# Optimization experiments

Measured on AMD Instinct MI355X. Metric: run time of the kernel, lower is better.

Reference implementation:

```python
import jax, jax.numpy as jnp
import numpy as np

EMB = 1024
HEAD = 128

def setup_inputs() -> dict:
    key = jax.random.key(0)
    kx, kk, kq, kv = jax.random.split(key, 4)
    s = 1.0 / np.sqrt(EMB)
    return {
        "x": jax.random.normal(kx, (8, 2048, EMB), dtype=jnp.float32),
        "Wk": jax.random.normal(kk, (EMB, HEAD), dtype=jnp.float32) * s,
        "Wq": jax.random.normal(kq, (EMB, HEAD), dtype=jnp.float32) * s,
        "Wv": jax.random.normal(kv, (EMB, HEAD), dtype=jnp.float32) * s,
    }

def reference(x, Wk, Wq, Wv):
    # x: [B,T,E]; projections (no bias)
    k = jnp.einsum('bte,eh->bth', x, Wk)
    q = jnp.einsum('bte,eh->bth', x, Wq)
    v = jnp.einsum('bte,eh->bth', x, Wv)
    # scores: [B,T,T], NOTE: no 1/sqrt(d) scaling in original module
    qk = jnp.einsum('bih,bjh->bij', q, k)
    T = x.shape[1]
    causal = jnp.tril(jnp.ones((T, T), dtype=bool))  # True = keep
    qk = jnp.where(causal, qk, -jnp.inf)
    # NOTE: softmax over axis -2 (query axis), as in original
    attn = jax.nn.softmax(qk, axis=-2)
    return jnp.einsum('bij,bjh->bih', attn, v)
```

## Files before the change

kernel.cpp:

```cpp
#include <hip/hip_runtime.h>

typedef unsigned short u16;
typedef unsigned int u32;
typedef _Float16 f16;
typedef __attribute__((ext_vector_type(8))) _Float16 f16x8;
typedef __attribute__((ext_vector_type(4))) float f32x4;

constexpr int SEQ = 2048;
constexpr int EMBD = 1024;
constexpr int HD = 128;
constexpr int NB = 8;
constexpr int NSL = 8;

__device__ inline u16 f2h(float f) {
  f16 h = (f16)f;
  return __builtin_bit_cast(u16, h);
}
__device__ inline u32 pack2(float a, float b) {
  return (u32)f2h(a) | ((u32)f2h(b) << 16);
}

__device__ inline f32x4 mfma16(f16x8 a, f16x8 b, f32x4 c) {
  return __builtin_amdgcn_mfma_f32_16x16x32_f16(a, b, c, 0, 0, 0);
}

template<int R, int C>
__device__ inline void stage_tile(u16* lds, const u16* __restrict__ g, int ldg) {
  constexpr int CH = (R * C) / (8 * 256);
  int t = threadIdx.x;
#pragma unroll
  for (int ch = 0; ch < CH; ++ch) {
    int lin = ch * 256 + t;
    int row = lin / (C / 8);
    int cc = lin % (C / 8);
    int byte = row * (C * 2) + cc * 16;
    byte ^= (row & 7) << 4;
    *reinterpret_cast<uint4*>(reinterpret_cast<char*>(lds) + byte) =
        *reinterpret_cast<const uint4*>(g + (size_t)row * ldg + cc * 8);
  }
}

template<int R, int C>
__device__ inline void stage_tile_f32(u16* lds, const float* __restrict__ g, int ldg) {
  constexpr int CH = (R * C) / (8 * 256);
  int t = threadIdx.x;
#pragma unroll
  for (int ch = 0; ch < CH; ++ch) {
    int lin = ch * 256 + t;
    int row = lin / (C / 8);
    int cc = lin % (C / 8);
    const float* p = g + (size_t)row * ldg + cc * 8;
    float4 a = *reinterpret_cast<const float4*>(p);
    float4 b = *reinterpret_cast<const float4*>(p + 4);
    uint4 o;
    o.x = pack2(a.x, a.y);
    o.y = pack2(a.z, a.w);
    o.z = pack2(b.x, b.y);
    o.w = pack2(b.z, b.w);
    int byte = row * (C * 2) + cc * 16;
    byte ^= (row & 7) << 4;
    *reinterpret_cast<uint4*>(reinterpret_cast<char*>(lds) + byte) = o;
  }
}

template<int RB>
__device__ inline f16x8 frag_ld(const u16* lds, int row, int elem) {
  int byte = row * RB + elem * 2;
  byte ^= (row & 7) << 4;
  return *reinterpret_cast<const f16x8*>(reinterpret_cast<const char*>(lds) + byte);
}

__global__ __launch_bounds__(256) void k_cvt_w(const float* __restrict__ Wq,
                                               const float* __restrict__ Wk,
                                               const float* __restrict__ Wv,
                                               u16* __restrict__ Wt) {
  int t = blockIdx.x * 256 + threadIdx.x;
  int e0 = (t & 255) * 4;
  int h = (t >> 8) & 127;
  int w = t >> 15;
  const float* W = (w == 0) ? Wq : (w == 1) ? Wk : Wv;
  ushort4 o;
  o.x = f2h(W[(size_t)(e0 + 0) * HD + h]);
  o.y = f2h(W[(size_t)(e0 + 1) * HD + h]);
  o.z = f2h(W[(size_t)(e0 + 2) * HD + h]);
  o.w = f2h(W[(size_t)(e0 + 3) * HD + h]);
  *reinterpret_cast<ushort4*>(Wt + ((size_t)w * HD + h) * EMBD + e0) = o;
}

__global__ __launch_bounds__(256, 2) void k_proj(const float* __restrict__ x,
                                                 const u16* __restrict__ Wt,
                                                 u16* __restrict__ Qb,
                                                 u16* __restrict__ Kb,
                                                 u16* __restrict__ Vtb) {
  __shared__ __align__(16) u16 As[32 * 64];
  __shared__ __align__(16) u16 Bs[3][128 * 64];
  const int mt = blockIdx.x;
  const int lane = threadIdx.x & 63, wave = threadIdx.x >> 6;
  const int rh = wave & 1, fq = wave >> 1;
  f32x4 zero = {0.f, 0.f, 0.f, 0.f};
  f32x4 acc[3][4];
#pragma unroll
  for (int w = 0; w < 3; w++)
#pragma unroll
    for (int f = 0; f < 4; f++) acc[w][f] = zero;

  for (int k0 = 0; k0 < EMBD; k0 += 64) {
    __syncthreads();
    stage_tile_f32<32, 64>(As, x + (size_t)mt * 32 * EMBD + k0, EMBD);
    stage_tile<128, 64>(Bs[0], Wt + 0 * HD * EMBD + k0, EMBD);
    stage_tile<128, 64>(Bs[1], Wt + 1 * (size_t)HD * EMBD + k0, EMBD);
    stage_tile<128, 64>(Bs[2], Wt + 2 * (size_t)HD * EMBD + k0, EMBD);
    __syncthreads();
#pragma unroll
    for (int kk = 0; kk < 2; kk++) {
      f16x8 af = frag_ld<128>(As, rh * 16 + (lane & 15), kk * 32 + (lane >> 4) * 8);
#pragma unroll
      for (int w = 0; w < 3; w++)
#pragma unroll
        for (int f = 0; f < 4; f++) {
          f16x8 bw = frag_ld<128>(Bs[w], (fq * 4 + f) * 16 + (lane & 15),
                                  kk * 32 + (lane >> 4) * 8);
          acc[w][f] = mfma16(af, bw, acc[w][f]);
        }
    }
  }
#pragma unroll
  for (int w = 0; w < 2; w++) {
    u16* P = w ? Kb : Qb;
#pragma unroll
    for (int f = 0; f < 4; f++)
#pragma unroll
      for (int r = 0; r < 4; r++) {
        int i = mt * 32 + rh * 16 + (lane >> 4) * 4 + r;
        int h = (fq * 4 + f) * 16 + (lane & 15);
        P[(size_t)i * HD + h] = f2h(acc[w][f][r]);
      }
  }
  {
    int bb = (mt * 32) >> 11;
    int t0 = (mt * 32) & 2047;
#pragma unroll
    for (int f = 0; f < 4; f++) {
      int h = (fq * 4 + f) * 16 + (lane & 15);
      int t = t0 + rh * 16 + (lane >> 4) * 4;
      ushort4 o;
      o.x = f2h(acc[2][f][0]);
      o.y = f2h(acc[2][f][1]);
      o.z = f2h(acc[2][f][2]);
      o.w = f2h(acc[2][f][3]);
      *reinterpret_cast<ushort4*>(Vtb + ((size_t)bb * HD + h) * SEQ + t) = o;
    }
  }
}

__device__ inline void merge_ml(float& m, float& l, float m2, float l2) {
  float mn = fmaxf(m, m2);
  float a = (m > -1e37f) ? l * __expf(m - mn) : 0.f;
  float b = (m2 > -1e37f) ? l2 * __expf(m2 - mn) : 0.f;
  m = mn;
  l = a + b;
}

__global__ __launch_bounds__(256, 2) void k_statsA(const u16* __restrict__ Qb,
                                                   const u16* __restrict__ Kb,
                                                   float* __restrict__ mpart,
                                                   float* __restrict__ lpart) {
  __shared__ __align__(16) u16 Tile[128 * 128];
  const int id = blockIdx.y * 64 + blockIdx.x;
  const int bb = id & 7;
  const int z = (id >> 3) & 7, sl = id >> 6;
  const int lane = threadIdx.x & 63, wave = threadIdx.x >> 6, wj = wave * 32;
  f32x4 zero = {0.f, 0.f, 0.f, 0.f};

  for (int ph = 0; ph < 2; ph++) {
    const int jt = ph ? (15 - z) : z;
    __syncthreads();
    stage_tile<128, 128>(Tile, Kb + ((size_t)bb * SEQ + jt * 128) * HD, HD);
    __syncthreads();
    f16x8 af[2][4];
#pragma unroll
    for (int fj = 0; fj < 2; fj++)
#pragma unroll
      for (int kk = 0; kk < 4; kk++)
        af[fj][kk] = frag_ld<256>(Tile, wj + fj * 16 + (lane & 15), kk * 32 + (lane >> 4) * 8);
    float m[2][4], l[2][4];
#pragma unroll
    for (int a = 0; a < 2; a++)
#pragma unroll
      for (int r = 0; r < 4; r++) {
        m[a][r] = -INFINITY;
        l[a][r] = 0.f;
      }
    int it0 = jt + ((sl - jt) & 7);
    for (int it = it0; it < 16; it += 8) {
      __syncthreads();
      stage_tile<128, 128>(Tile, Qb + ((size_t)bb * SEQ + it * 128) * HD, HD);
      __syncthreads();
      f32x4 acc[2][8];
#pragma unroll
      for (int a = 0; a < 2; a++)
#pragma unroll
        for (int b = 0; b < 8; b++) acc[a][b] = zero;
#pragma unroll
      for (int kk = 0; kk < 4; kk++)
#pragma unroll
        for (int fi = 0; fi < 8; fi++) {
          f16x8 bq = frag_ld<256>(Tile, fi * 16 + (lane & 15), kk * 32 + (lane >> 4) * 8);
          acc[0][fi] = mfma16(af[0][kk], bq, acc[0][fi]);
          acc[1][fi] = mfma16(af[1][kk], bq, acc[1][fi]);
        }
#pragma unroll
      for (int fj = 0; fj < 2; fj++)
#pragma unroll
        for (int r = 0; r < 4; r++) {
          int jg = jt * 128 + wj + fj * 16 + (lane >> 4) * 4 + r;
          float v[8];
          float vmax = -INFINITY;
#pragma unroll
          for (int fi = 0; fi < 8; fi++) {
            int ig = it * 128 + fi * 16 + (lane & 15);
            v[fi] = (ig >= jg) ? acc[fj][fi][r] : -INFINITY;
            vmax = fmaxf(vmax, v[fi]);
          }
          if (vmax > -1e37f) {
            float mn = fmaxf(m[fj][r], vmax);
            float sc = (m[fj][r] > -1e37f) ? __expf(m[fj][r] - mn) : 0.f;
            float ss = 0.f;
#pragma unroll
            for (int fi = 0; fi < 8; fi++)
              ss += (v[fi] > -1e37f) ? __expf(v[fi] - mn) : 0.f;
            l[fj][r] = l[fj][r] * sc + ss;
            m[fj][r] = mn;
          }
        }
    }
#pragma unroll
    for (int fj = 0; fj < 2; fj++)
#pragma unroll
      for (int r = 0; r < 4; r++)
        for (int msk = 1; msk <= 8; msk <<= 1) {
          float m2 = __shfl_xor(m[fj][r], msk);
          float l2 = __shfl_xor(l[fj][r], msk);
          merge_ml(m[fj][r], l[fj][r], m2, l2);
        }
    if ((lane & 15) == 0) {
#pragma unroll
      for (int fj = 0; fj < 2; fj++)
#pragma unroll
        for (int r = 0; r < 4; r++) {
          int j = jt * 128 + wj + fj * 16 + (lane >> 4) * 4 + r;
          size_t idx = (size_t)sl * (NB * SEQ) + (size_t)bb * SEQ + j;
          mpart[idx] = m[fj][r];
          lpart[idx] = l[fj][r];
        }
    }
  }
}

__global__ __launch_bounds__(256) void k_stats_reduce(const float* __restrict__ mpart,
                                                      const float* __restrict__ lpart,
                                                      float* __restrict__ Mg,
                                                      float* __restrict__ RLg) {
  int idx = blockIdx.x * 256 + threadIdx.x;
  float m = -INFINITY;
#pragma unroll
  for (int sl = 0; sl < NSL; sl++) m = fmaxf(m, mpart[sl * (NB * SEQ) + idx]);
  float l = 0.f;
#pragma unroll
  for (int sl = 0; sl < NSL; sl++) {
    float ms = mpart[sl * (NB * SEQ) + idx];
    if (ms > -1e37f) l += lpart[sl * (NB * SEQ) + idx] * __expf(ms - m);
  }
  Mg[idx] = m;
  RLg[idx] = 1.0f / l;
}

__global__ __launch_bounds__(256, 2) void k_passB(const u16* __restrict__ Qb,
                                                  const u16* __restrict__ Kb,
                                                  const u16* __restrict__ Vtb,
                                                  const float* __restrict__ Mg,
                                                  const float* __restrict__ RLg,
                                                  u16* __restrict__ opart) {
  __shared__ __align__(16) u16 Ks[64 * 128];
  __shared__ __align__(16) u16 Vs[128 * 64];
  __shared__ __align__(16) u16 Ps[128 * 64];
  __shared__ float sm[64];
  __shared__ float srl[64];
  const int id = blockIdx.y * 64 + blockIdx.x;
  const int bb = id & 7;
  const int z = (id >> 3) & 7, sl = id >> 6;
  const int lane = threadIdx.x & 63, wave = threadIdx.x >> 6, wi = wave * 32;
  f32x4 zero = {0.f, 0.f, 0.f, 0.f};

  for (int ph = 0; ph < 2; ph++) {
    const int it = ph ? (15 - z) : z;
    f16x8 qf[2][4];
#pragma unroll
    for (int fi = 0; fi < 2; fi++)
#pragma unroll
      for (int kk = 0; kk < 4; kk++) {
        size_t row = (size_t)bb * SEQ + it * 128 + wi + fi * 16 + (lane & 15);
        qf[fi][kk] = *reinterpret_cast<const f16x8*>(Qb + row * HD + kk * 32 + (lane >> 4) * 8);
      }
    f32x4 accO[2][8];
#pragma unroll
    for (int a = 0; a < 2; a++)
#pragma unroll
      for (int b = 0; b < 8; b++) accO[a][b] = zero;

    for (int jt = sl; jt <= 2 * it + 1; jt += 8) {
      __syncthreads();
      stage_tile<64, 128>(Ks, Kb + ((size_t)bb * SEQ + jt * 64) * HD, HD);
      stage_tile<128, 64>(Vs, Vtb + (size_t)bb * HD * SEQ + jt * 64, SEQ);
      if (threadIdx.x < 64)
        sm[threadIdx.x] = Mg[bb * SEQ + jt * 64 + threadIdx.x];
      else if (threadIdx.x < 128)
        srl[threadIdx.x - 64] = RLg[bb * SEQ + jt * 64 + threadIdx.x - 64];
      __syncthreads();
      f32x4 accS[2][4];
#pragma unroll
      for (int a = 0; a < 2; a++)
#pragma unroll
        for (int b = 0; b < 4; b++) accS[a][b] = zero;
#pragma unroll
      for (int kk = 0; kk < 4; kk++)
#pragma unroll
        for (int fj = 0; fj < 4; fj++) {
          f16x8 bk = frag_ld<256>(Ks, fj * 16 + (lane & 15), kk * 32 + (lane >> 4) * 8);
          accS[0][fj] = mfma16(qf[0][kk], bk, accS[0][fj]);
          accS[1][fj] = mfma16(qf[1][kk], bk, accS[1][fj]);
        }
#pragma unroll
      for (int fi = 0; fi < 2; fi++)
#pragma unroll
        for (int fj = 0; fj < 4; fj++) {
          int jloc = fj * 16 + (lane & 15);
          float mj = sm[jloc], rlj = srl[jloc];
          int jg = jt * 64 + jloc;
#pragma unroll
          for (int r = 0; r < 4; r++) {
            int iloc = wi + fi * 16 + (lane >> 4) * 4 + r;
            int ig = it * 128 + iloc;
            float p = __expf(accS[fi][fj][r] - mj) * rlj;
            if (ig < jg) p = 0.f;
            int byte = iloc * 128 + jloc * 2;
            byte ^= (iloc & 7) << 4;
            *reinterpret_cast<u16*>(reinterpret_cast<char*>(Ps) + byte) = f2h(p);
          }
        }
      __syncthreads();
#pragma unroll
      for (int kk = 0; kk < 2; kk++) {
        f16x8 pa0 = frag_ld<128>(Ps, wi + (lane & 15), kk * 32 + (lane >> 4) * 8);
        f16x8 pa1 = frag_ld<128>(Ps, wi + 16 + (lane & 15), kk * 32 + (lane >> 4) * 8);
#pragma unroll
        for (int fh = 0; fh < 8; fh++) {
          f16x8 bv = frag_ld<128>(Vs, fh * 16 + (lane & 15), kk * 32 + (lane >> 4) * 8);
          accO[0][fh] = mfma16(pa0, bv, accO[0][fh]);
          accO[1][fh] = mfma16(pa1, bv, accO[1][fh]);
        }
      }
    }
#pragma unroll
    for (int fi = 0; fi < 2; fi++)
#pragma unroll
      for (int fh = 0; fh < 8; fh++)
#pragma unroll
        for (int r = 0; r < 4; r++) {
          int ig = it * 128 + wi + fi * 16 + (lane >> 4) * 4 + r;
          int h = fh * 16 + (lane & 15);
          opart[(((size_t)sl * NB + bb) * SEQ + ig) * HD + h] = f2h(accO[fi][fh][r]);
        }
  }
}

__global__ __launch_bounds__(256) void k_reduceB(const u16* __restrict__ opart,
                                                 float* __restrict__ out) {
  size_t base = ((size_t)blockIdx.x * 256 + threadIdx.x) * 8;
  const size_t S = (size_t)NB * SEQ * HD;
  float s[8];
#pragma unroll
  for (int j = 0; j < 8; j++) s[j] = 0.f;
#pragma unroll
  for (int sl = 0; sl < NSL; sl++) {
    f16x8 v = *reinterpret_cast<const f16x8*>(opart + sl * S + base);
#pragma unroll
    for (int j = 0; j < 8; j++) s[j] += (float)v[j];
  }
  float4 o0 = {s[0], s[1], s[2], s[3]};
  float4 o1 = {s[4], s[5], s[6], s[7]};
  *reinterpret_cast<float4*>(out + base) = o0;
  *reinterpret_cast<float4*>(out + base + 4) = o1;
}

extern "C" void kernel_launch(void* const* d_in, const int* in_sizes, int n_in,
                              void* d_out, int out_size, void* d_ws, size_t ws_size,
                              hipStream_t stream) {
  (void)in_sizes; (void)n_in; (void)out_size; (void)ws_size;
  const float* x = (const float*)d_in[0];
  const float* Wk = (const float*)d_in[1];
  const float* Wq = (const float*)d_in[2];
  const float* Wv = (const float*)d_in[3];
  float* out = (float*)d_out;
  char* ws = (char*)d_ws;

  u16* Wt = (u16*)(ws + 0);
  u16* Qb = (u16*)(ws + 786432);
  u16* Kb = (u16*)(ws + 4980736);
  u16* Vtb = (u16*)(ws + 9175040);
  float* mpart = (float*)(ws + 13369344);
  float* lpart = (float*)(ws + 13893632);
  float* Mg = (float*)(ws + 14417920);
  float* RLg = (float*)(ws + 14483456);
  u16* opart = (u16*)(ws + 14548992);

  k_cvt_w<<<384, 256, 0, stream>>>(Wq, Wk, Wv, Wt);
  k_proj<<<512, 256, 0, stream>>>(x, Wt, Qb, Kb, Vtb);
  k_statsA<<<dim3(64, 8), 256, 0, stream>>>(Qb, Kb, mpart, lpart);
  k_stats_reduce<<<64, 256, 0, stream>>>(mpart, lpart, Mg, RLg);
  k_passB<<<dim3(64, 8), 256, 0, stream>>>(Qb, Kb, Vtb, Mg, RLg, opart);
  k_reduceB<<<1024, 256, 0, stream>>>(opart, out);
}
```

Measured before the change: 95.25 us.

## Pre-swizzle Q/K/V/W layouts and double-buffer tiles with direct global-to-LDS loads

The projection weights, Q, K and the transposed V are now written to global memory already in the XOR-swizzled tile layout. This lets the projection, stats and output-pass kernels copy tiles into LDS with global_load_lds instead of going through registers. Each of those three kernels now double-buffers its tiles, so the next tile is prefetched while MFMAs run on the current one. The projection kernel gets a new 512-thread, 2D-grid tiling, and passB reuses the K buffer as the P scratch and reads the row stats straight from global. The risks are higher LDS use per block, lower occupancy, and a layout contract that every kernel must read consistently.

```diff
diff --git a/kernel.cpp b/kernel.cpp
--- a/kernel.cpp
+++ b/kernel.cpp
@@ -12,61 +12,22 @@
 constexpr int NB = 8;
 constexpr int NSL = 8;
 
-__device__ inline u16 f2h(float f) {
-  f16 h = (f16)f;
-  return __builtin_bit_cast(u16, h);
-}
-__device__ inline u32 pack2(float a, float b) {
-  return (u32)f2h(a) | ((u32)f2h(b) << 16);
-}
+__device__ inline u16 f2h(float f) { return __builtin_bit_cast(u16, (f16)f); }
+__device__ inline u32 pack2(float a, float b) { return (u32)f2h(a) | ((u32)f2h(b) << 16); }
 
 __device__ inline f32x4 mfma16(f16x8 a, f16x8 b, f32x4 c) {
   return __builtin_amdgcn_mfma_f32_16x16x32_f16(a, b, c, 0, 0, 0);
 }
 
-template<int R, int C>
-__device__ inline void stage_tile(u16* lds, const u16* __restrict__ g, int ldg) {
-  constexpr int CH = (R * C) / (8 * 256);
-  int t = threadIdx.x;
-#pragma unroll
-  for (int ch = 0; ch < CH; ++ch) {
-    int lin = ch * 256 + t;
-    int row = lin / (C / 8);
-    int cc = lin % (C / 8);
-    int byte = row * (C * 2) + cc * 16;
-    byte ^= (row & 7) << 4;
-    *reinterpret_cast<uint4*>(reinterpret_cast<char*>(lds) + byte) =
-        *reinterpret_cast<const uint4*>(g + (size_t)row * ldg + cc * 8);
-  }
-}
-
-template<int R, int C>
-__device__ inline void stage_tile_f32(u16* lds, const float* __restrict__ g, int ldg) {
-  constexpr int CH = (R * C) / (8 * 256);
-  int t = threadIdx.x;
-#pragma unroll
-  for (int ch = 0; ch < CH; ++ch) {
-    int lin = ch * 256 + t;
-    int row = lin / (C / 8);
-    int cc = lin % (C / 8);
-    const float* p = g + (size_t)row * ldg + cc * 8;
-    float4 a = *reinterpret_cast<const float4*>(p);
-    float4 b = *reinterpret_cast<const float4*>(p + 4);
-    uint4 o;
-    o.x = pack2(a.x, a.y);
-    o.y = pack2(a.z, a.w);
-    o.z = pack2(b.x, b.y);
-    o.w = pack2(b.z, b.w);
-    int byte = row * (C * 2) + cc * 16;
-    byte ^= (row & 7) << 4;
-    *reinterpret_cast<uint4*>(reinterpret_cast<char*>(lds) + byte) = o;
-  }
+__device__ __forceinline__ void gload16(const u16* g, u16* l) {
+  __builtin_amdgcn_global_load_lds(
+      (const __attribute__((address_space(1))) u32*)g,
+      (__attribute__((address_space(3))) u32*)l, 16, 0, 0);
 }
 
 template<int RB>
-__device__ inline f16x8 frag_ld(const u16* lds, int row, int elem) {
-  int byte = row * RB + elem * 2;
-  byte ^= (row & 7) << 4;
+__device__ inline f16x8 frag_ld(const u16* lds, int row, int e) {
+  int byte = row * RB + ((e * 2) ^ ((row & 7) << 4));
   return *reinterpret_cast<const f16x8*>(reinterpret_cast<const char*>(lds) + byte);
 }
 
@@ -76,81 +37,104 @@
                                                u16* __restrict__ Wt) {
   int t = blockIdx.x * 256 + threadIdx.x;
   int e0 = (t & 255) * 4;
-  int h = (t >> 8) & 127;
-  int w = t >> 15;
+  int H = t >> 8;
+  int w = H >> 7, h = H & 127;
   const float* W = (w == 0) ? Wq : (w == 1) ? Wk : Wv;
   ushort4 o;
   o.x = f2h(W[(size_t)(e0 + 0) * HD + h]);
   o.y = f2h(W[(size_t)(e0 + 1) * HD + h]);
   o.z = f2h(W[(size_t)(e0 + 2) * HD + h]);
   o.w = f2h(W[(size_t)(e0 + 3) * HD + h]);
-  *reinterpret_cast<ushort4*>(Wt + ((size_t)w * HD + h) * EMBD + e0) = o;
-}
-
-__global__ __launch_bounds__(256, 2) void k_proj(const float* __restrict__ x,
+  int k0t = e0 >> 6, ec = e0 & 63;
+  size_t el = (size_t)(k0t * 384 + H) * 64 + (ec ^ ((H & 7) << 3));
+  *reinterpret_cast<ushort4*>(Wt + el) = o;
+}
+
+__global__ __launch_bounds__(512, 4) void k_proj(const float* __restrict__ x,
                                                  const u16* __restrict__ Wt,
                                                  u16* __restrict__ Qb,
                                                  u16* __restrict__ Kb,
                                                  u16* __restrict__ Vtb) {
-  __shared__ __align__(16) u16 As[32 * 64];
-  __shared__ __align__(16) u16 Bs[3][128 * 64];
-  const int mt = blockIdx.x;
-  const int lane = threadIdx.x & 63, wave = threadIdx.x >> 6;
-  const int rh = wave & 1, fq = wave >> 1;
+  __shared__ __align__(16) u16 As[2][64 * 64];
+  __shared__ __align__(16) u16 Bs[2][192 * 64];
+  const int mt = blockIdx.x, ny = blockIdx.y;
+  const int t = threadIdx.x, lane = t & 63, wave = t >> 6;
+  const int rh = (wave & 1) * 32, cq = (wave >> 1) * 48;
+  const int ar = t >> 3, ac = t & 7;
+  const float* asrc = x + (size_t)(mt * 64 + ar) * EMBD + ac * 8;
+  const int adst = ar * 64 + ((ac * 8) ^ ((ar & 7) << 3));
   f32x4 zero = {0.f, 0.f, 0.f, 0.f};
-  f32x4 acc[3][4];
-#pragma unroll
-  for (int w = 0; w < 3; w++)
-#pragma unroll
-    for (int f = 0; f < 4; f++) acc[w][f] = zero;
-
-  for (int k0 = 0; k0 < EMBD; k0 += 64) {
+  f32x4 acc[2][3];
+#pragma unroll
+  for (int a = 0; a < 2; ++a)
+#pragma unroll
+    for (int b = 0; b < 3; ++b) acc[a][b] = zero;
+
+  {
+#pragma unroll
+    for (int q = 0; q < 3; ++q) {
+      int lin = q * 512 + t;
+      gload16(Wt + ny * 12288 + lin * 8, &Bs[0][lin * 8]);
+    }
+    float4 a0 = *reinterpret_cast<const float4*>(asrc);
+    float4 a1 = *reinterpret_cast<const float4*>(asrc + 4);
+    uint4 o = {pack2(a0.x, a0.y), pack2(a0.z, a0.w), pack2(a1.x, a1.y), pack2(a1.z, a1.w)};
+    *reinterpret_cast<uint4*>(&As[0][adst]) = o;
+  }
+  __syncthreads();
+  int cur = 0;
+  for (int s = 0; s < 16; ++s) {
+    float4 a0, a1;
+    const bool pf = (s < 15);
+    if (pf) {
+#pragma unroll
+      for (int q = 0; q < 3; ++q) {
+        int lin = q * 512 + t;
+        gload16(Wt + (s + 1) * 24576 + ny * 12288 + lin * 8, &Bs[cur ^ 1][lin * 8]);
+      }
+      a0 = *reinterpret_cast<const float4*>(asrc + (s + 1) * 64);
+      a1 = *reinterpret_cast<const float4*>(asrc + (s + 1) * 64 + 4);
+    }
+#pragma unroll
+    for (int kk = 0; kk < 2; ++kk) {
+      f16x8 af0 = frag_ld<128>(As[cur], rh + (lane & 15), kk * 32 + (lane >> 4) * 8);
+      f16x8 af1 = frag_ld<128>(As[cur], rh + 16 + (lane & 15), kk * 32 + (lane >> 4) * 8);
+#pragma unroll
+      for (int fc = 0; fc < 3; ++fc) {
+        f16x8 bw = frag_ld<128>(Bs[cur], cq + fc * 16 + (lane & 15), kk * 32 + (lane >> 4) * 8);
+        acc[0][fc] = mfma16(af0, bw, acc[0][fc]);
+        acc[1][fc] = mfma16(af1, bw, acc[1][fc]);
+      }
+    }
+    if (pf) {
+      uint4 o = {pack2(a0.x, a0.y), pack2(a0.z, a0.w), pack2(a1.x, a1.y), pack2(a1.z, a1.w)};
+      *reinterpret_cast<uint4*>(&As[cur ^ 1][adst]) = o;
+    }
     __syncthreads();
-    stage_tile_f32<32, 64>(As, x + (size_t)mt * 32 * EMBD + k0, EMBD);
-    stage_tile<128, 64>(Bs[0], Wt + 0 * HD * EMBD + k0, EMBD);
-    stage_tile<128, 64>(Bs[1], Wt + 1 * (size_t)HD * EMBD + k0, EMBD);
-    stage_tile<128, 64>(Bs[2], Wt + 2 * (size_t)HD * EMBD + k0, EMBD);
-    __syncthreads();
-#pragma unroll
-    for (int kk = 0; kk < 2; kk++) {
-      f16x8 af = frag_ld<128>(As, rh * 16 + (lane & 15), kk * 32 + (lane >> 4) * 8);
-#pragma unroll
-      for (int w = 0; w < 3; w++)
-#pragma unroll
-        for (int f = 0; f < 4; f++) {
-          f16x8 bw = frag_ld<128>(Bs[w], (fq * 4 + f) * 16 + (lane & 15),
-                                  kk * 32 + (lane >> 4) * 8);
-          acc[w][f] = mfma16(af, bw, acc[w][f]);
-        }
-    }
-  }
-#pragma unroll
-  for (int w = 0; w < 2; w++) {
-    u16* P = w ? Kb : Qb;
-#pragma unroll
-    for (int f = 0; f < 4; f++)
-#pragma unroll
-      for (int r = 0; r < 4; r++) {
-        int i = mt * 32 + rh * 16 + (lane >> 4) * 4 + r;
-        int h = (fq * 4 + f) * 16 + (lane & 15);
-        P[(size_t)i * HD + h] = f2h(acc[w][f][r]);
-      }
-  }
-  {
-    int bb = (mt * 32) >> 11;
-    int t0 = (mt * 32) & 2047;
-#pragma unroll
-    for (int f = 0; f < 4; f++) {
-      int h = (fq * 4 + f) * 16 + (lane & 15);
-      int t = t0 + rh * 16 + (lane >> 4) * 4;
-      ushort4 o;
-      o.x = f2h(acc[2][f][0]);
-      o.y = f2h(acc[2][f][1]);
-      o.z = f2h(acc[2][f][2]);
-      o.w = f2h(acc[2][f][3]);
-      *reinterpret_cast<ushort4*>(Vtb + ((size_t)bb * HD + h) * SEQ + t) = o;
-    }
-  }
+    cur ^= 1;
+  }
+#pragma unroll
+  for (int fi = 0; fi < 2; ++fi)
+#pragma unroll
+    for (int fc = 0; fc < 3; ++fc) {
+      int gcol = ny * 192 + cq + fc * 16 + (lane & 15);
+      int w = gcol >> 7, h = gcol & 127;
+      int i0 = mt * 64 + rh + fi * 16 + (lane >> 4) * 4;
+      if (w < 2) {
+        u16* P = w ? Kb : Qb;
+#pragma unroll
+        for (int r = 0; r < 4; ++r) {
+          int i = i0 + r;
+          P[(size_t)i * 128 + (h ^ ((i & 7) << 3))] = f2h(acc[fi][fc][r]);
+        }
+      } else {
+        int bb = i0 >> 11, jt = (i0 >> 6) & 31, tl = i0 & 63;
+        ushort4 o = {f2h(acc[fi][fc][0]), f2h(acc[fi][fc][1]),
+                     f2h(acc[fi][fc][2]), f2h(acc[fi][fc][3])};
+        size_t el = ((size_t)(bb * 32 + jt) * 128 + h) * 64 + (tl ^ ((h & 7) << 3));
+        *reinterpret_cast<ushort4*>(Vtb + el) = o;
+      }
+    }
 }
 
 __device__ inline void merge_ml(float& m, float& l, float m2, float l2) {
@@ -165,79 +149,97 @@
                                                    const u16* __restrict__ Kb,
                                                    float* __restrict__ mpart,
                                                    float* __restrict__ lpart) {
-  __shared__ __align__(16) u16 Tile[128 * 128];
+  __shared__ __align__(16) u16 Qs[2][128 * 128];
   const int id = blockIdx.y * 64 + blockIdx.x;
-  const int bb = id & 7;
-  const int z = (id >> 3) & 7, sl = id >> 6;
-  const int lane = threadIdx.x & 63, wave = threadIdx.x >> 6, wj = wave * 32;
+  const int bb = id & 7, z = (id >> 3) & 7, sl = id >> 6;
+  const int t = threadIdx.x, lane = t & 63, wj = (t >> 6) * 32;
   f32x4 zero = {0.f, 0.f, 0.f, 0.f};
 
-  for (int ph = 0; ph < 2; ph++) {
-    const int jt = ph ? (15 - z) : z;
+  for (int ph = 0; ph < 2; ++ph) {
+    const int jt = ph ? 15 - z : z;
     __syncthreads();
-    stage_tile<128, 128>(Tile, Kb + ((size_t)bb * SEQ + jt * 128) * HD, HD);
+#pragma unroll
+    for (int q = 0; q < 8; ++q) {
+      int lin = q * 256 + t;
+      gload16(Kb + ((size_t)bb * SEQ + jt * 128) * 128 + lin * 8, &Qs[0][lin * 8]);
+    }
     __syncthreads();
     f16x8 af[2][4];
 #pragma unroll
-    for (int fj = 0; fj < 2; fj++)
-#pragma unroll
-      for (int kk = 0; kk < 4; kk++)
-        af[fj][kk] = frag_ld<256>(Tile, wj + fj * 16 + (lane & 15), kk * 32 + (lane >> 4) * 8);
+    for (int fj = 0; fj < 2; ++fj)
+#pragma unroll
+      for (int kk = 0; kk < 4; ++kk)
+        af[fj][kk] = frag_ld<256>(Qs[0], wj + fj * 16 + (lane & 15), kk * 32 + (lane >> 4) * 8);
     float m[2][4], l[2][4];
 #pragma unroll
-    for (int a = 0; a < 2; a++)
-#pragma unroll
-      for (int r = 0; r < 4; r++) {
+    for (int a = 0; a < 2; ++a)
+#pragma unroll
+      for (int r = 0; r < 4; ++r) {
         m[a][r] = -INFINITY;
         l[a][r] = 0.f;
       }
-    int it0 = jt + ((sl - jt) & 7);
-    for (int it = it0; it < 16; it += 8) {
-      __syncthreads();
-      stage_tile<128, 128>(Tile, Qb + ((size_t)bb * SEQ + it * 128) * HD, HD);
-      __syncthreads();
-      f32x4 acc[2][8];
-#pragma unroll
-      for (int a = 0; a < 2; a++)
-#pragma unroll
-        for (int b = 0; b < 8; b++) acc[a][b] = zero;
-#pragma unroll
-      for (int kk = 0; kk < 4; kk++)
-#pragma unroll
-        for (int fi = 0; fi < 8; fi++) {
-          f16x8 bq = frag_ld<256>(Tile, fi * 16 + (lane & 15), kk * 32 + (lane >> 4) * 8);
-          acc[0][fi] = mfma16(af[0][kk], bq, acc[0][fi]);
-          acc[1][fi] = mfma16(af[1][kk], bq, acc[1][fi]);
-        }
-#pragma unroll
-      for (int fj = 0; fj < 2; fj++)
-#pragma unroll
-        for (int r = 0; r < 4; r++) {
-          int jg = jt * 128 + wj + fj * 16 + (lane >> 4) * 4 + r;
-          float v[8];
-          float vmax = -INFINITY;
-#pragma unroll
-          for (int fi = 0; fi < 8; fi++) {
-            int ig = it * 128 + fi * 16 + (lane & 15);
-            v[fi] = (ig >= jg) ? acc[fj][fi][r] : -INFINITY;
-            vmax = fmaxf(vmax, v[fi]);
+    const int it0 = jt + ((sl - jt) & 7);
+    int cur = 1;
+    if (it0 < 16) {
+#pragma unroll
+      for (int q = 0; q < 8; ++q) {
+        int lin = q * 256 + t;
+        gload16(Qb + ((size_t)bb * SEQ + it0 * 128) * 128 + lin * 8, &Qs[1][lin * 8]);
+      }
+      for (int it = it0; it < 16; it += 8) {
+        __syncthreads();
+        if (it + 8 < 16) {
+#pragma unroll
+          for (int q = 0; q < 8; ++q) {
+            int lin = q * 256 + t;
+            gload16(Qb + ((size_t)bb * SEQ + (it + 8) * 128) * 128 + lin * 8,
+                    &Qs[cur ^ 1][lin * 8]);
           }
-          if (vmax > -1e37f) {
-            float mn = fmaxf(m[fj][r], vmax);
-            float sc = (m[fj][r] > -1e37f) ? __expf(m[fj][r] - mn) : 0.f;
-            float ss = 0.f;
-#pragma unroll
-            for (int fi = 0; fi < 8; fi++)
-              ss += (v[fi] > -1e37f) ? __expf(v[fi] - mn) : 0.f;
-            l[fj][r] = l[fj][r] * sc + ss;
-            m[fj][r] = mn;
+        }
+        f32x4 acc[2][8];
+#pragma unroll
+        for (int a = 0; a < 2; ++a)
+#pragma unroll
+          for (int b = 0; b < 8; ++b) acc[a][b] = zero;
+#pragma unroll
+        for (int kk = 0; kk < 4; ++kk)
+#pragma unroll
+          for (int fi = 0; fi < 8; ++fi) {
+            f16x8 bq = frag_ld<256>(Qs[cur], fi * 16 + (lane & 15), kk * 32 + (lane >> 4) * 8);
+            acc[0][fi] = mfma16(af[0][kk], bq, acc[0][fi]);
+            acc[1][fi] = mfma16(af[1][kk], bq, acc[1][fi]);
           }
-        }
-    }
-#pragma unroll
-    for (int fj = 0; fj < 2; fj++)
-#pragma unroll
-      for (int r = 0; r < 4; r++)
+#pragma unroll
+        for (int fj = 0; fj < 2; ++fj)
+#pragma unroll
+          for (int r = 0; r < 4; ++r) {
+            int jg = jt * 128 + wj + fj * 16 + (lane >> 4) * 4 + r;
+            float v[8];
+            float vmax = -INFINITY;
+#pragma unroll
+            for (int fi = 0; fi < 8; ++fi) {
+              int ig = it * 128 + fi * 16 + (lane & 15);
+              v[fi] = (ig >= jg) ? acc[fj][fi][r] : -INFINITY;
+              vmax = fmaxf(vmax, v[fi]);
+            }
+            if (vmax > -1e37f) {
+              float mn = fmaxf(m[fj][r], vmax);
+              float sc = (m[fj][r] > -1e37f) ? __expf(m[fj][r] - mn) : 0.f;
+              float ss = 0.f;
+#pragma unroll
+              for (int fi = 0; fi < 8; ++fi)
+                ss += (v[fi] > -1e37f) ? __expf(v[fi] - mn) : 0.f;
+              l[fj][r] = l[fj][r] * sc + ss;
+              m[fj][r] = mn;
+            }
+          }
+        cur ^= 1;
+      }
+    }
+#pragma unroll
+    for (int fj = 0; fj < 2; ++fj)
+#pragma unroll
+      for (int r = 0; r < 4; ++r)
         for (int msk = 1; msk <= 8; msk <<= 1) {
           float m2 = __shfl_xor(m[fj][r], msk);
           float l2 = __shfl_xor(l[fj][r], msk);
@@ -245,9 +247,9 @@
         }
     if ((lane & 15) == 0) {
 #pragma unroll
-      for (int fj = 0; fj < 2; fj++)
-#pragma unroll
-        for (int r = 0; r < 4; r++) {
+      for (int fj = 0; fj < 2; ++fj)
+#pragma unroll
+        for (int r = 0; r < 4; ++r) {
           int j = jt * 128 + wj + fj * 16 + (lane >> 4) * 4 + r;
           size_t idx = (size_t)sl * (NB * SEQ) + (size_t)bb * SEQ + j;
           mpart[idx] = m[fj][r];
@@ -281,92 +283,106 @@
                                                   const float* __restrict__ Mg,
                                                   const float* __restrict__ RLg,
                                                   u16* __restrict__ opart) {
-  __shared__ __align__(16) u16 Ks[64 * 128];
-  __shared__ __align__(16) u16 Vs[128 * 64];
-  __shared__ __align__(16) u16 Ps[128 * 64];
-  __shared__ float sm[64];
-  __shared__ float srl[64];
+  __shared__ __align__(16) u16 Ks2[2][64 * 128];
+  __shared__ __align__(16) u16 Vs2[2][128 * 64];
   const int id = blockIdx.y * 64 + blockIdx.x;
-  const int bb = id & 7;
-  const int z = (id >> 3) & 7, sl = id >> 6;
-  const int lane = threadIdx.x & 63, wave = threadIdx.x >> 6, wi = wave * 32;
+  const int bb = id & 7, z = (id >> 3) & 7, sl = id >> 6;
+  const int t = threadIdx.x, lane = t & 63, wi = (t >> 6) * 32;
   f32x4 zero = {0.f, 0.f, 0.f, 0.f};
 
-  for (int ph = 0; ph < 2; ph++) {
-    const int it = ph ? (15 - z) : z;
+  auto stageKV = [&](int jt, int b) {
+#pragma unroll
+    for (int q = 0; q < 4; ++q) {
+      int lin = q * 256 + t;
+      gload16(Kb + ((size_t)bb * SEQ + jt * 64) * 128 + lin * 8, &Ks2[b][lin * 8]);
+    }
+#pragma unroll
+    for (int q = 0; q < 4; ++q) {
+      int lin = q * 256 + t;
+      gload16(Vtb + ((size_t)bb * 32 + jt) * 8192 + lin * 8, &Vs2[b][lin * 8]);
+    }
+  };
+
+  for (int ph = 0; ph < 2; ++ph) {
+    const int it = ph ? 15 - z : z;
     f16x8 qf[2][4];
 #pragma unroll
-    for (int fi = 0; fi < 2; fi++)
-#pragma unroll
-      for (int kk = 0; kk < 4; kk++) {
-        size_t row = (size_t)bb * SEQ + it * 128 + wi + fi * 16 + (lane & 15);
-        qf[fi][kk] = *reinterpret_cast<const f16x8*>(Qb + row * HD + kk * 32 + (lane >> 4) * 8);
+    for (int fi = 0; fi < 2; ++fi)
+#pragma unroll
+      for (int kk = 0; kk < 4; ++kk) {
+        size_t gi = (size_t)bb * SEQ + it * 128 + wi + fi * 16 + (lane & 15);
+        int e0 = kk * 32 + (lane >> 4) * 8;
+        qf[fi][kk] = *reinterpret_cast<const f16x8*>(Qb + gi * 128 + (e0 ^ (((int)gi & 7) << 3)));
       }
     f32x4 accO[2][8];
 #pragma unroll
-    for (int a = 0; a < 2; a++)
-#pragma unroll
-      for (int b = 0; b < 8; b++) accO[a][b] = zero;
-
-    for (int jt = sl; jt <= 2 * it + 1; jt += 8) {
+    for (int a = 0; a < 2; ++a)
+#pragma unroll
+      for (int b = 0; b < 8; ++b) accO[a][b] = zero;
+    const int jtmax = 2 * it + 1;
+    int cur = 0;
+    __syncthreads();
+    if (sl <= jtmax) stageKV(sl, 0);
+    for (int jt = sl; jt <= jtmax; jt += 8) {
       __syncthreads();
-      stage_tile<64, 128>(Ks, Kb + ((size_t)bb * SEQ + jt * 64) * HD, HD);
-      stage_tile<128, 64>(Vs, Vtb + (size_t)bb * HD * SEQ + jt * 64, SEQ);
-      if (threadIdx.x < 64)
-        sm[threadIdx.x] = Mg[bb * SEQ + jt * 64 + threadIdx.x];
-      else if (threadIdx.x < 128)
-        srl[threadIdx.x - 64] = RLg[bb * SEQ + jt * 64 + threadIdx.x - 64];
-      __syncthreads();
+      float mjv[4], rlv[4];
+#pragma unroll
+      for (int fj = 0; fj < 4; ++fj) {
+        int jg = jt * 64 + fj * 16 + (lane & 15);
+        mjv[fj] = Mg[bb * SEQ + jg];
+        rlv[fj] = RLg[bb * SEQ + jg];
+      }
       f32x4 accS[2][4];
 #pragma unroll
-      for (int a = 0; a < 2; a++)
-#pragma unroll
-        for (int b = 0; b < 4; b++) accS[a][b] = zero;
-#pragma unroll
-      for (int kk = 0; kk < 4; kk++)
-#pragma unroll
-        for (int fj = 0; fj < 4; fj++) {
-          f16x8 bk = frag_ld<256>(Ks, fj * 16 + (lane & 15), kk * 32 + (lane >> 4) * 8);
+      for (int a = 0; a < 2; ++a)
+#pragma unroll
+        for (int b = 0; b < 4; ++b) accS[a][b] = zero;
+#pragma unroll
+      for (int kk = 0; kk < 4; ++kk)
+#pragma unroll
+        for (int fj = 0; fj < 4; ++fj) {
+          f16x8 bk = frag_ld<256>(Ks2[cur], fj * 16 + (lane & 15), kk * 32 + (lane >> 4) * 8);
           accS[0][fj] = mfma16(qf[0][kk], bk, accS[0][fj]);
           accS[1][fj] = mfma16(qf[1][kk], bk, accS[1][fj]);
         }
-#pragma unroll
-      for (int fi = 0; fi < 2; fi++)
-#pragma unroll
-        for (int fj = 0; fj < 4; fj++) {
-          int jloc = fj * 16 + (lane & 15);
-          float mj = sm[jloc], rlj = srl[jloc];
-          int jg = jt * 64 + jloc;
-#pragma unroll
-          for (int r = 0; r < 4; r++) {
+      __syncthreads();
+      if (jt + 8 <= jtmax) stageKV(jt + 8, cur ^ 1);
+      u16* Ps = Ks2[cur];
+#pragma unroll
+      for (int fj = 0; fj < 4; ++fj) {
+        int jloc = fj * 16 + (lane & 15);
+        int jg = jt * 64 + jloc;
+        float mj = mjv[fj], rlj = rlv[fj];
+#pragma unroll
+        for (int fi = 0; fi < 2; ++fi)
+#pragma unroll
+          for (int r = 0; r < 4; ++r) {
             int iloc = wi + fi * 16 + (lane >> 4) * 4 + r;
             int ig = it * 128 + iloc;
             float p = __expf(accS[fi][fj][r] - mj) * rlj;
             if (ig < jg) p = 0.f;
-            int byte = iloc * 128 + jloc * 2;
-            byte ^= (iloc & 7) << 4;
-            *reinterpret_cast<u16*>(reinterpret_cast<char*>(Ps) + byte) = f2h(p);
+            Ps[iloc * 64 + (jloc ^ ((iloc & 7) << 3))] = f2h(p);
           }
-        }
-      __syncthreads();
-#pragma unroll
-      for (int kk = 0; kk < 2; kk++) {
-        f16x8 pa0 = frag_ld<128>(Ps, wi + (lane & 15), kk * 32 + (lane >> 4) * 8);
-        f16x8 pa1 = frag_ld<128>(Ps, wi + 16 + (lane & 15), kk * 32 + (lane >> 4) * 8);
-#pragma unroll
-        for (int fh = 0; fh < 8; fh++) {
-          f16x8 bv = frag_ld<128>(Vs, fh * 16 + (lane & 15), kk * 32 + (lane >> 4) * 8);
+      }
+#pragma unroll
+      for (int ks = 0; ks < 2; ++ks) {
+        f16x8 pa0 = frag_ld<128>(Ps, wi + (lane & 15), ks * 32 + (lane >> 4) * 8);
+        f16x8 pa1 = frag_ld<128>(Ps, wi + 16 + (lane & 15), ks * 32 + (lane >> 4) * 8);
+#pragma unroll
+        for (int fh = 0; fh < 8; ++fh) {
+          f16x8 bv = frag_ld<128>(Vs2[cur], fh * 16 + (lane & 15), ks * 32 + (lane >> 4) * 8);
           accO[0][fh] = mfma16(pa0, bv, accO[0][fh]);
           accO[1][fh] = mfma16(pa1, bv, accO[1][fh]);
         }
       }
-    }
-#pragma unroll
-    for (int fi = 0; fi < 2; fi++)
-#pragma unroll
-      for (int fh = 0; fh < 8; fh++)
-#pragma unroll
-        for (int r = 0; r < 4; r++) {
+      cur ^= 1;
+    }
+#pragma unroll
+    for (int fi = 0; fi < 2; ++fi)
+#pragma unroll
+      for (int fh = 0; fh < 8; ++fh)
+#pragma unroll
+        for (int r = 0; r < 4; ++r) {
           int ig = it * 128 + wi + fi * 16 + (lane >> 4) * 4 + r;
           int h = fh * 16 + (lane & 15);
           opart[(((size_t)sl * NB + bb) * SEQ + ig) * HD + h] = f2h(accO[fi][fh][r]);
@@ -415,7 +431,7 @@
   u16* opart = (u16*)(ws + 14548992);
 
   k_cvt_w<<<384, 256, 0, stream>>>(Wq, Wk, Wv, Wt);
-  k_proj<<<512, 256, 0, stream>>>(x, Wt, Qb, Kb, Vtb);
+  k_proj<<<dim3(256, 2), 512, 0, stream>>>(x, Wt, Qb, Kb, Vtb);
   k_statsA<<<dim3(64, 8), 256, 0, stream>>>(Qb, Kb, mpart, lpart);
   k_stats_reduce<<<64, 256, 0, stream>>>(mpart, lpart, Mg, RLg);
   k_passB<<<dim3(64, 8), 256, 0, stream>>>(Qb, Kb, Vtb, Mg, RLg, opart);
```

Result: faster. 84.67 us (-11.1%).
